# Kernel optimization log

Hardware: AMD Instinct MI355X
Metric: run time of the kernel (lower is better)

The kernel has to match this reference:

```python
import jax, jax.numpy as jnp
import numpy as np

H = 16          # num heads
D = 128         # head dim
WIN = 128       # local sliding window
EPS = 1e-6
ROPE_BASE = 500000.0


def rmsnorm(x, w, eps=EPS):
    var = jnp.mean(x * x, axis=-1, keepdims=True)
    return x * jax.lax.rsqrt(var + eps) * w


def rope(x, positions):
    # x: [T, H, D], neox-style rotate-halves
    half = D // 2
    inv_freq = 1.0 / (ROPE_BASE ** (jnp.arange(half, dtype=jnp.float32) / half * 2.0 / 2.0 * 2.0))
    inv_freq = 1.0 / (ROPE_BASE ** (jnp.arange(0, D, 2, dtype=jnp.float32) / D))
    ang = positions.astype(jnp.float32)[:, None] * inv_freq[None, :]      # [T, D/2]
    cos, sin = jnp.cos(ang)[:, None, :], jnp.sin(ang)[:, None, :]         # [T, 1, D/2]
    x1, x2 = x[..., :half], x[..., half:]
    return jnp.concatenate([x1 * cos - x2 * sin, x2 * cos + x1 * sin], axis=-1)


def attend(q, k, v, mask, scale):
    # q,k,v: [T, H, D]; mask: [T, T] (True = attend)
    scores = jnp.einsum('thd,shd->hts', q, k) * scale
    scores = jnp.where(mask[None], scores, jnp.finfo(scores.dtype).min)
    p = jax.nn.softmax(scores, axis=-1)
    return jnp.einsum('hts,shd->thd', p, v)


def setup_inputs() -> dict:
    key = jax.random.key(0)
    ks = jax.random.split(key, 8)
    T, hid = 2048, 2048
    s = 0.02
    return {
        'hidden_states': jax.random.normal(ks[0], (T, hid), jnp.float32),
        'positions': jnp.arange(T, dtype=jnp.int32),
        'Wq': jax.random.normal(ks[1], (hid, H * D + H), jnp.float32) * s,
        'Wk': jax.random.normal(ks[2], (hid, H * D), jnp.float32) * s,
        'Wv': jax.random.normal(ks[3], (hid, H * D), jnp.float32) * s,
        'Wo': jax.random.normal(ks[4], (H * D, hid), jnp.float32) * s,
        'q_norm_w': jnp.ones((hid,), jnp.float32),
        'k_norm_w': jnp.ones((H * D,), jnp.float32),
    }


def reference(hidden_states, positions, Wq, Wk, Wv, Wo, q_norm_w, k_norm_w):
    T = hidden_states.shape[0]
    scale = D ** -0.5
    qg = hidden_states @ Wq                             # [T, H*D + H]
    q, gate = qg[:, :H * D], qg[:, H * D:]              # [T, H*D], [T, H]
    k = hidden_states @ Wk
    v = hidden_states @ Wv
    q = rmsnorm(q, q_norm_w)
    k = rmsnorm(k, k_norm_w)
    q = rope(q.reshape(T, H, D), positions)
    k = rope(k.reshape(T, H, D), positions)
    v = v.reshape(T, H, D)
    # masks
    pi, pj = positions[:, None], positions[None, :]
    causal = pi >= pj
    local = causal & ((pi - pj) < WIN)
    global_out = attend(q, k, v, causal, scale)         # [T, H, D]
    local_out = attend(q, k, v, local, scale)           # [T, H, D]
    gate_hard = (jax.nn.sigmoid(gate) > 0.5).astype(hidden_states.dtype)[:, :, None]
    blended = global_out * gate_hard + local_out * (1.0 - gate_hard)
    return blended.reshape(T, H * D) @ Wo
```

## Files before the change

kernel.cpp:

```cpp
#include <hip/hip_runtime.h>

typedef _Float16 f16;
typedef __attribute__((ext_vector_type(8))) _Float16 half8;
typedef __attribute__((ext_vector_type(4))) _Float16 half4v;
typedef __attribute__((ext_vector_type(4))) float floatx4;

#define T_DIM 2048
#define HID   2048
#define NH    16
#define HD    128
#define QG_LD 2064
#define SM_SCALE 0.08838834764831845f
#define NEG_BIG  -1e30f

__device__ __forceinline__ void async16(const void* g, void* l) {
  __builtin_amdgcn_global_load_lds((const __attribute__((address_space(1))) void*)g,
                                   (__attribute__((address_space(3))) void*)l, 16, 0, 0);
}

__global__ __launch_bounds__(256) void transpose_all(const float* __restrict__ Wq,
                                                     const float* __restrict__ Wk,
                                                     const float* __restrict__ Wv,
                                                     f16* __restrict__ WqT, f16* __restrict__ WkT,
                                                     f16* __restrict__ WvT) {
  __shared__ float tile[32][33];
  const int z = blockIdx.z;
  const float* src = (z == 0) ? Wq : ((z == 1) ? Wk : Wv);
  const int ld = (z == 0) ? QG_LD : 2048;
  f16* dst = (z == 0) ? WqT : ((z == 1) ? WkT : WvT);
  const int bx = blockIdx.x * 32, by = blockIdx.y * 32;
  const int tx = threadIdx.x, ty = threadIdx.y;
#pragma unroll
  for (int i = 0; i < 4; ++i)
    tile[ty + 8 * i][tx] = src[(size_t)(by + ty + 8 * i) * ld + bx + tx];
  __syncthreads();
#pragma unroll
  for (int i = 0; i < 4; ++i)
    dst[(size_t)(bx + ty + 8 * i) * HID + by + tx] = (f16)tile[tx][ty + 8 * i];
}

__global__ __launch_bounds__(256) void transpose_w(const float* __restrict__ src, int src_ld,
                                                   f16* __restrict__ dst) {
  __shared__ float tile[32][33];
  const int bx = blockIdx.x * 32, by = blockIdx.y * 32;
  const int tx = threadIdx.x, ty = threadIdx.y;
#pragma unroll
  for (int i = 0; i < 4; ++i)
    tile[ty + 8 * i][tx] = src[(size_t)(by + ty + 8 * i) * src_ld + bx + tx];
  __syncthreads();
#pragma unroll
  for (int i = 0; i < 4; ++i)
    dst[(size_t)(bx + ty + 8 * i) * HID + by + tx] = (f16)tile[tx][ty + 8 * i];
}

__global__ __launch_bounds__(256) void transpose_h(const f16* __restrict__ src, f16* __restrict__ dst) {
  __shared__ f16 tile[32][33];
  const int bx = blockIdx.x * 32, by = blockIdx.y * 32;
  const int tx = threadIdx.x, ty = threadIdx.y;
#pragma unroll
  for (int i = 0; i < 4; ++i)
    tile[ty + 8 * i][tx] = src[(size_t)(by + ty + 8 * i) * T_DIM + bx + tx];
  __syncthreads();
#pragma unroll
  for (int i = 0; i < 4; ++i)
    dst[(size_t)(bx + ty + 8 * i) * T_DIM + by + tx] = tile[tx][ty + 8 * i];
}

__global__ __launch_bounds__(256) void convert_f32_f16(const float* __restrict__ src, f16* __restrict__ dst) {
  const int i = (blockIdx.x * 256 + threadIdx.x) * 4;
  const float4 v = *(const float4*)(src + i);
  half4v o;
  o.x = (f16)v.x; o.y = (f16)v.y; o.z = (f16)v.z; o.w = (f16)v.w;
  *(half4v*)(dst + i) = o;
}

__global__ __launch_bounds__(256) void gate_kernel(const float* __restrict__ hidden,
                                                   const float* __restrict__ Wq,
                                                   float* __restrict__ gate) {
  __shared__ double red[256][16];
  const int t = blockIdx.x, tid = threadIdx.x;
  double sums[16];
#pragma unroll
  for (int h2 = 0; h2 < 16; ++h2) sums[h2] = 0.0;
  const float* hrow = hidden + (size_t)t * HID;
  for (int k = tid; k < HID; k += 256) {
    const double hv = (double)hrow[k];
    const float* wr = Wq + (size_t)k * QG_LD + 2048;
#pragma unroll
    for (int h2 = 0; h2 < 16; ++h2) sums[h2] += hv * (double)wr[h2];
  }
#pragma unroll
  for (int h2 = 0; h2 < 16; ++h2) red[tid][h2] = sums[h2];
  __syncthreads();
  for (int st = 128; st > 0; st >>= 1) {
    if (tid < st) {
#pragma unroll
      for (int h2 = 0; h2 < 16; ++h2) red[tid][h2] += red[tid + st][h2];
    }
    __syncthreads();
  }
  if (tid < 16) gate[(size_t)t * 16 + tid] = (red[0][tid] > 0.0) ? 1.f : 0.f;
}

__global__ __launch_bounds__(256) void norm_rope2(const f16* __restrict__ qsrc, const f16* __restrict__ ksrc,
                                                  const float* __restrict__ qw, const float* __restrict__ kw,
                                                  const int* __restrict__ pos,
                                                  f16* __restrict__ qdst, f16* __restrict__ kdst) {
  __shared__ float row[2048];
  __shared__ float red[256];
  const int t = blockIdx.x & 2047, sel = blockIdx.x >> 11, tid = threadIdx.x;
  const f16* s = (sel ? ksrc : qsrc) + (size_t)t * HID;
  const float* w = sel ? kw : qw;
  f16* dst = sel ? kdst : qdst;
  float ss = 0.f;
#pragma unroll
  for (int e = 0; e < 8; ++e) {
    float v = (float)s[tid + 256 * e];
    row[tid + 256 * e] = v;
    ss += v * v;
  }
  red[tid] = ss;
  __syncthreads();
  for (int st = 128; st > 0; st >>= 1) {
    if (tid < st) red[tid] += red[tid + st];
    __syncthreads();
  }
  const float scl = rsqrtf(red[0] * (1.f / 2048.f) + 1e-6f);
  const float p = (float)pos[t];
#pragma unroll
  for (int e = 0; e < 8; ++e) {
    const int idx = tid + 256 * e;
    const int d = idx & 127;
    const int dh = d & 63;
    const int pidx = (d < 64) ? idx + 64 : idx - 64;
    const float xn = row[idx] * scl * w[idx];
    const float xp = row[pidx] * scl * w[pidx];
    const float inv = __expf(-(float)dh * 0.20503692772194388f);
    float cs, sn;
    sincosf(p * inv, &sn, &cs);
    const float o = (d < 64) ? (xn * cs - xp * sn) : (xn * cs + xp * sn);
    dst[(size_t)t * HID + idx] = (f16)o;
  }
}

__device__ __forceinline__ void gemm_issue(const f16* __restrict__ A, const f16* __restrict__ Bt,
                                           char* As, char* Bs, int m0, int n0, int k0,
                                           int wave, int srow, int scol) {
#pragma unroll
  for (int i = 0; i < 4; ++i) {
    async16(A + (size_t)(m0 + 32 * i + srow) * 2048 + k0 + scol, As + 4096 * i + 1024 * wave);
    async16(Bt + (size_t)(n0 + 32 * i + srow) * 2048 + k0 + scol, Bs + 4096 * i + 1024 * wave);
  }
}

__device__ __forceinline__ void gemm_core_db(const f16* __restrict__ A, const f16* __restrict__ Bt,
                                             f16* As, f16* Bs, floatx4 (&acc)[4][4],
                                             int kbase, int klen) {
  const int tid = threadIdx.x;
  const int lane = tid & 63, wave = tid >> 6;
  const int m0 = blockIdx.y * 128, n0 = blockIdx.x * 128;
  const int mo = (wave >> 1) * 64, no = (wave & 1) * 64;
  const int cn = lane & 15, q16 = lane >> 4;
  const int srow = 8 * wave + (lane >> 3);
  const int scol = (lane & 7) * 8;
  gemm_issue(A, Bt, (char*)As, (char*)Bs, m0, n0, kbase, wave, srow, scol);
  int cur = 0;
  for (int k0 = kbase; k0 < kbase + klen; k0 += 64) {
    __syncthreads();
    if (k0 + 64 < kbase + klen)
      gemm_issue(A, Bt, (char*)(As + (cur ^ 1) * 8192), (char*)(Bs + (cur ^ 1) * 8192),
                 m0, n0, k0 + 64, wave, srow, scol);
    const f16* as = As + cur * 8192;
    const f16* bs = Bs + cur * 8192;
#pragma unroll
    for (int kk = 0; kk < 64; kk += 32) {
      half8 av[4], bv[4];
#pragma unroll
      for (int i = 0; i < 4; ++i) av[i] = *(const half8*)&as[(mo + i * 16 + cn) * 64 + kk + q16 * 8];
#pragma unroll
      for (int i = 0; i < 4; ++i) bv[i] = *(const half8*)&bs[(no + i * 16 + cn) * 64 + kk + q16 * 8];
#pragma unroll
      for (int i = 0; i < 4; ++i)
#pragma unroll
        for (int j = 0; j < 4; ++j)
          acc[i][j] = __builtin_amdgcn_mfma_f32_16x16x32_f16(av[i], bv[j], acc[i][j], 0, 0, 0);
    }
    cur ^= 1;
  }
}

#define NKT 32

__device__ __forceinline__ void stage_half(const f16* __restrict__ src, int row0, int kcol,
                                           char* dst, int wv, int lane) {
  const int rsw = lane >> 3;
  const int csw = ((lane & 7) ^ rsw) << 3;
#pragma unroll
  for (int L = 0; L < 2; ++L)
    async16(src + (size_t)(row0 + L * 64 + wv * 8 + rsw) * 2048 + kcol + csw,
            dst + (L * 64 + wv * 8) * 128);
}

template <int MQ>
__device__ __forceinline__ void ld_a4(half8 (&a)[4][2], const f16* As, int wm, int cn, int q16) {
#pragma unroll
  for (int rf = 0; rf < 4; ++rf)
#pragma unroll
    for (int kh = 0; kh < 2; ++kh) {
      const int R = wm * 128 + MQ * 64 + rf * 16 + cn;
      a[rf][kh] = *(const half8*)&As[R * 64 + (((kh * 4 + q16) ^ (cn & 7)) << 3)];
    }
}

template <int NQ>
__device__ __forceinline__ void ld_b2(half8 (&b)[2][2], const f16* Bs, int wn, int cn, int q16) {
#pragma unroll
  for (int cf = 0; cf < 2; ++cf)
#pragma unroll
    for (int kh = 0; kh < 2; ++kh) {
      const int S = wn * 64 + NQ * 32 + cf * 16 + cn;
      b[cf][kh] = *(const half8*)&Bs[S * 64 + (((kh * 4 + q16) ^ (cn & 7)) << 3)];
    }
}

template <int MQ, int NQ>
__device__ __forceinline__ void mma16(floatx4 (&acc)[8][4], const half8 (&a)[4][2], const half8 (&b)[2][2]) {
#pragma unroll
  for (int kh = 0; kh < 2; ++kh)
#pragma unroll
    for (int rf = 0; rf < 4; ++rf)
#pragma unroll
      for (int cf = 0; cf < 2; ++cf)
        acc[MQ * 4 + rf][NQ * 2 + cf] = __builtin_amdgcn_mfma_f32_16x16x32_f16(
            a[rf][kh], b[cf][kh], acc[MQ * 4 + rf][NQ * 2 + cf], 0, 0, 0);
}

#define LGKM0() asm volatile("s_waitcnt lgkmcnt(0)" ::: "memory")
#define BAR()   __builtin_amdgcn_s_barrier()
#define PRIO(x) __builtin_amdgcn_s_setprio(x)
#define HBASE(p, isB, h) ((char*)lds + (p) * 65536 + (isB) * 32768 + (h) * 16384)

__global__ __launch_bounds__(512, 2) void gemm_qkv8(const f16* __restrict__ A,
                                                    const f16* __restrict__ B0_, const f16* __restrict__ B1_,
                                                    const f16* __restrict__ B2_,
                                                    f16* __restrict__ C0, f16* __restrict__ C1,
                                                    f16* __restrict__ C2) {
  __shared__ __align__(16) f16 lds[65536];
  const int tid = threadIdx.x;
  const int lane = tid & 63, wv = tid >> 6;
  const int wm = wv >> 2, wn = wv & 3;
  const int q16 = lane >> 4, cn = lane & 15;
  const int z = blockIdx.z;
  const f16* Bt = (z == 0) ? B0_ : ((z == 1) ? B1_ : B2_);
  f16* C = (z == 0) ? C0 : ((z == 1) ? C1 : C2);
  const int m0 = blockIdx.y * 256, n0 = blockIdx.x * 256;

  floatx4 acc[8][4] = {};
  half8 a[4][2], b0[2][2], b1[2][2];

  stage_half(A,  m0,       0,  HBASE(0, 0, 0), wv, lane);
  stage_half(Bt, n0,       0,  HBASE(0, 1, 0), wv, lane);
  stage_half(Bt, n0 + 128, 0,  HBASE(0, 1, 1), wv, lane);
  stage_half(A,  m0 + 128, 0,  HBASE(0, 0, 1), wv, lane);
  stage_half(Bt, n0,       64, HBASE(1, 1, 0), wv, lane);
  stage_half(A,  m0,       64, HBASE(1, 0, 0), wv, lane);
  asm volatile("s_waitcnt vmcnt(4)" ::: "memory");
  BAR();

  for (int t = 0; t < NKT; ++t) {
    const int pb = t & 1;
    const f16* As = lds + pb * 32768;
    const f16* Bs = As + 16384;
    ld_a4<0>(a, As, wm, cn, q16);
    ld_b2<0>(b0, Bs, wn, cn, q16);
    if (t + 1 < NKT) stage_half(Bt, n0 + 128, (t + 1) * 64, HBASE(pb ^ 1, 1, 1), wv, lane);
    LGKM0(); BAR();
    PRIO(1); mma16<0, 0>(acc, a, b0); PRIO(0);
    BAR();
    ld_b2<1>(b1, Bs, wn, cn, q16);
    if (t + 1 < NKT) stage_half(A, m0 + 128, (t + 1) * 64, HBASE(pb ^ 1, 0, 1), wv, lane);
    LGKM0(); BAR();
    PRIO(1); mma16<0, 1>(acc, a, b1); PRIO(0);
    BAR();
    ld_a4<1>(a, As, wm, cn, q16);
    if (t + 2 < NKT) stage_half(Bt, n0, (t + 2) * 64, HBASE(pb, 1, 0), wv, lane);
    LGKM0(); BAR();
    PRIO(1); mma16<1, 0>(acc, a, b0); PRIO(0);
    BAR();
    if (t + 2 < NKT) {
      stage_half(A, m0, (t + 2) * 64, HBASE(pb, 0, 0), wv, lane);
      asm volatile("s_waitcnt vmcnt(4)" ::: "memory");
    } else if (t == NKT - 2) {
      asm volatile("s_waitcnt vmcnt(0)" ::: "memory");
    }
    BAR();
    PRIO(1); mma16<1, 1>(acc, a, b1); PRIO(0);
    BAR();
  }

  const int r0 = q16 * 4;
#pragma unroll
  for (int i = 0; i < 8; ++i)
#pragma unroll
    for (int j = 0; j < 4; ++j)
#pragma unroll
      for (int r = 0; r < 4; ++r)
        C[(size_t)(m0 + wm * 128 + i * 16 + r0 + r) * 2048 + n0 + wn * 64 + j * 16 + cn] =
            (f16)acc[i][j][r];
}

__global__ __launch_bounds__(256, 2) void gemm_out_sk(const f16* __restrict__ A, const f16* __restrict__ Bt,
                                                      float* __restrict__ P0, float* __restrict__ P1) {
  __shared__ __align__(16) f16 As[2 * 128 * 64];
  __shared__ __align__(16) f16 Bs[2 * 128 * 64];
  const int z = blockIdx.z;
  floatx4 acc[4][4] = {};
  gemm_core_db(A, Bt, As, Bs, acc, z * 1024, 1024);
  float* C = z ? P1 : P0;
  const int lane = threadIdx.x & 63, wave = threadIdx.x >> 6;
  const int mb = blockIdx.y * 128 + (wave >> 1) * 64;
  const int nb = blockIdx.x * 128 + (wave & 1) * 64;
  const int r0 = (lane >> 4) * 4, cn = lane & 15;
#pragma unroll
  for (int i = 0; i < 4; ++i)
#pragma unroll
    for (int j = 0; j < 4; ++j)
#pragma unroll
      for (int r = 0; r < 4; ++r)
        C[(size_t)(mb + i * 16 + r0 + r) * 2048 + nb + j * 16 + cn] = acc[i][j][r];
}

__global__ __launch_bounds__(256) void add_out(const float* __restrict__ P0, const float* __restrict__ P1,
                                               float* __restrict__ out) {
  const int i = (blockIdx.x * 256 + threadIdx.x) * 4;
  const float4 a = *(const float4*)(P0 + i);
  const float4 b = *(const float4*)(P1 + i);
  float4 o;
  o.x = a.x + b.x; o.y = a.y + b.y; o.z = a.z + b.z; o.w = a.w + b.w;
  *(float4*)(out + i) = o;
}

__global__ __launch_bounds__(256, 2) void flash_kernel(const f16* __restrict__ Qg, const f16* __restrict__ Kg,
                                                       const f16* __restrict__ VTg, const float* __restrict__ gate,
                                                       f16* __restrict__ Oa) {
  __shared__ __align__(16) f16 Ks[2][64 * 128];
  __shared__ __align__(16) f16 VTs[2][128 * 64];
  __shared__ __align__(16) f16 Ps[4][16][72];

  const int tid = threadIdx.x;
  const int lane = tid & 63, wv = tid >> 6;
  const int q16 = lane >> 4, cn = lane & 15;
  const int r0 = q16 * 4;

  const int p = blockIdx.x;
  const int xcd = p & 7;
  const int idx = p >> 3;
  const int h = (xcd << 1) | (idx & 1);
  const int rest = idx >> 1;
  const int qt = (rest < 16) ? rest : 47 - rest;
  const int t0 = qt * 64;

  bool gbit[4];
#pragma unroll
  for (int r = 0; r < 4; ++r)
    gbit[r] = gate[(size_t)(t0 + wv * 16 + r0 + r) * NH + h] > 0.5f;

  half8 qa[4];
#pragma unroll
  for (int i = 0; i < 4; ++i)
    qa[i] = *(const half8*)(Qg + (size_t)(t0 + 16 * wv + cn) * HID + h * HD + 32 * i + q16 * 8);

#pragma unroll
  for (int i = 0; i < 4; ++i) {
    const int rk = 16 * i + 4 * wv + q16;
    async16(Kg + (size_t)rk * HID + h * HD + ((cn ^ (rk & 7)) << 3), (char*)Ks[0] + 4096 * i + 1024 * wv);
    const int rv = 32 * i + 8 * wv + (lane >> 3);
    async16(VTg + (size_t)(h * HD + rv) * T_DIM + (((lane & 7) ^ (lane >> 3)) << 3),
            (char*)VTs[0] + 4096 * i + 1024 * wv);
  }

  floatx4 og[8] = {};
  floatx4 lacc = {0.f, 0.f, 0.f, 0.f};
  float mg[4];
#pragma unroll
  for (int r = 0; r < 4; ++r) mg[r] = NEG_BIG;

  const half8 ones = {(f16)1, (f16)1, (f16)1, (f16)1, (f16)1, (f16)1, (f16)1, (f16)1};

  int cur = 0;
  for (int kt = 0; kt <= qt; ++kt) {
    const int s0 = kt * 64;
    __syncthreads();
    if (kt < qt) {
      const int sn = s0 + 64;
#pragma unroll
      for (int i = 0; i < 4; ++i) {
        const int rk = 16 * i + 4 * wv + q16;
        async16(Kg + (size_t)(sn + rk) * HID + h * HD + ((cn ^ (rk & 7)) << 3),
                (char*)Ks[cur ^ 1] + 4096 * i + 1024 * wv);
        const int rv = 32 * i + 8 * wv + (lane >> 3);
        async16(VTg + (size_t)(h * HD + rv) * T_DIM + sn + (((lane & 7) ^ (lane >> 3)) << 3),
                (char*)VTs[cur ^ 1] + 4096 * i + 1024 * wv);
      }
    }

    floatx4 sacc[4] = {};
    PRIO(1);
#pragma unroll
    for (int i = 0; i < 4; ++i)
#pragma unroll
      for (int nt = 0; nt < 4; ++nt) {
        half8 b = *(const half8*)&Ks[cur][(nt * 16 + cn) * 128 + (((4 * i + q16) ^ (cn & 7)) << 3)];
        sacc[nt] = __builtin_amdgcn_mfma_f32_16x16x32_f16(qa[i], b, sacc[nt], 0, 0, 0);
      }
    PRIO(0);

    const bool diag = (kt == qt);

    float pe[4][4];
#pragma unroll
    for (int nt = 0; nt < 4; ++nt)
#pragma unroll
      for (int r = 0; r < 4; ++r) {
        float x = sacc[nt][r] * SM_SCALE;
        if (diag && (s0 + nt * 16 + cn > t0 + wv * 16 + r0 + r)) x = NEG_BIG;
        pe[nt][r] = x;
      }

    float rmax[4];
#pragma unroll
    for (int r = 0; r < 4; ++r)
      rmax[r] = fmaxf(fmaxf(pe[0][r], pe[1][r]), fmaxf(pe[2][r], pe[3][r]));
#pragma unroll
    for (int off = 1; off < 16; off <<= 1)
#pragma unroll
      for (int r = 0; r < 4; ++r) rmax[r] = fmaxf(rmax[r], __shfl_xor(rmax[r], off, 64));

    float alpha[4];
#pragma unroll
    for (int r = 0; r < 4; ++r) {
      const float mn = fmaxf(mg[r], rmax[r]);
      alpha[r] = __expf(mg[r] - mn);
      mg[r] = mn;
    }
#pragma unroll
    for (int dt = 0; dt < 8; ++dt)
#pragma unroll
      for (int r = 0; r < 4; ++r) og[dt][r] *= alpha[r];
#pragma unroll
    for (int r = 0; r < 4; ++r) lacc[r] *= alpha[r];

#pragma unroll
    for (int nt = 0; nt < 4; ++nt)
#pragma unroll
      for (int r = 0; r < 4; ++r) {
        const float e = __expf(pe[nt][r] - mg[r]);
        const int tt = t0 + wv * 16 + r0 + r;
        const int s = s0 + nt * 16 + cn;
        const bool keep = gbit[r] || (tt - s < 128);
        Ps[wv][r0 + r][nt * 16 + cn] = keep ? (f16)e : (f16)0.f;
      }

    PRIO(1);
#pragma unroll
    for (int kk = 0; kk < 64; kk += 32) {
      half8 a = *(const half8*)&Ps[wv][cn][kk + q16 * 8];
#pragma unroll
      for (int dt = 0; dt < 8; ++dt) {
        half8 b = *(const half8*)&VTs[cur][(dt * 16 + cn) * 64 + ((((kk >> 3) + q16) ^ (cn & 7)) << 3)];
        og[dt] = __builtin_amdgcn_mfma_f32_16x16x32_f16(a, b, og[dt], 0, 0, 0);
      }
      lacc = __builtin_amdgcn_mfma_f32_16x16x32_f16(a, ones, lacc, 0, 0, 0);
    }
    PRIO(0);
    cur ^= 1;
  }

#pragma unroll
  for (int dt = 0; dt < 8; ++dt)
#pragma unroll
    for (int r = 0; r < 4; ++r) {
      const float v = og[dt][r] / lacc[r];
      Oa[(size_t)(t0 + wv * 16 + r0 + r) * HID + h * HD + dt * 16 + cn] = (f16)v;
    }
}

extern "C" void kernel_launch(void* const* d_in, const int* in_sizes, int n_in,
                              void* d_out, int out_size, void* d_ws, size_t ws_size,
                              hipStream_t stream) {
  const float* hidden = (const float*)d_in[0];
  const int* pos = (const int*)d_in[1];
  const float* Wq = (const float*)d_in[2];
  const float* Wk = (const float*)d_in[3];
  const float* Wv = (const float*)d_in[4];
  const float* Wo = (const float*)d_in[5];
  const float* qw = (const float*)d_in[6];
  const float* kw = (const float*)d_in[7];

  char* ws = (char*)d_ws;
  const size_t MB = 1ull << 20;
  f16* WqT = (f16*)(ws + 0 * MB);
  f16* WkT = (f16*)(ws + 8 * MB);
  f16* WvT = (f16*)(ws + 16 * MB);
  f16* hidh = (f16*)(ws + 24 * MB);
  f16* q_raw = (f16*)(ws + 32 * MB);
  f16* k_raw = (f16*)(ws + 48 * MB);
  f16* v_h = (f16*)(ws + 64 * MB);
  f16* q_h = (f16*)(ws + 72 * MB);
  f16* k_h = (f16*)(ws + 80 * MB);
  float* gate = (float*)(ws + 88 * MB);
  f16* WoT = WqT;
  f16* attn = q_raw;
  f16* vT = k_raw;
  float* P0 = (float*)(ws + 8 * MB);
  float* P1 = (float*)(ws + 72 * MB);

  dim3 tb(32, 8);
  transpose_all<<<dim3(64, 64, 3), tb, 0, stream>>>(Wq, Wk, Wv, WqT, WkT, WvT);
  convert_f32_f16<<<4096, 256, 0, stream>>>(hidden, hidh);
  gate_kernel<<<2048, 256, 0, stream>>>(hidden, Wq, gate);
  gemm_qkv8<<<dim3(8, 8, 3), 512, 0, stream>>>(hidh, WqT, WkT, WvT, q_raw, k_raw, v_h);
  transpose_w<<<dim3(64, 64), tb, 0, stream>>>(Wo, 2048, WoT);
  norm_rope2<<<4096, 256, 0, stream>>>(q_raw, k_raw, qw, kw, pos, q_h, k_h);
  transpose_h<<<dim3(64, 64), tb, 0, stream>>>(v_h, vT);
  flash_kernel<<<512, 256, 0, stream>>>(q_h, k_h, vT, gate, attn);
  gemm_out_sk<<<dim3(16, 16, 2), 256, 0, stream>>>(attn, WoT, P0, P1);
  add_out<<<4096, 256, 0, stream>>>(P0, P1, (float*)d_out);
}
```

Measured before the change: 346.7 us.

## Split long causal query tiles across blocks and merge partial softmax results

Result: no change. 348.7 us (+0.6%).

```diff
diff --git a/kernel.cpp b/kernel.cpp
--- a/kernel.cpp
+++ b/kernel.cpp
@@ -342,7 +342,8 @@
 
 __global__ __launch_bounds__(256, 2) void flash_kernel(const f16* __restrict__ Qg, const f16* __restrict__ Kg,
                                                        const f16* __restrict__ VTg, const float* __restrict__ gate,
-                                                       f16* __restrict__ Oa) {
+                                                       f16* __restrict__ Oa, float* __restrict__ Opart,
+                                                       float2* __restrict__ ml) {
   __shared__ __align__(16) f16 Ks[2][64 * 128];
   __shared__ __align__(16) f16 VTs[2][128 * 64];
   __shared__ __align__(16) f16 Ps[4][16][72];
@@ -353,11 +354,18 @@
   const int r0 = q16 * 4;
 
   const int p = blockIdx.x;
-  const int xcd = p & 7;
-  const int idx = p >> 3;
-  const int h = (xcd << 1) | (idx & 1);
-  const int rest = idx >> 1;
-  const int qt = (rest < 16) ? rest : 47 - rest;
+  const int o = p >> 4;
+  const int h = p & 15;
+  int qt, nsp, piece, slot_o;
+  if (o < 24)      { qt = 31 - o / 3;        nsp = 3; piece = o % 3;        slot_o = o; }
+  else if (o < 36) { qt = 35 - o;            nsp = 1; piece = 0;            slot_o = 0; }
+  else             { int u = o - 36; qt = 23 - (u >> 1); nsp = 2; piece = u & 1; slot_o = 24 + u; }
+  const int L = qt + 1;
+  const int base = L / nsp, rem = L % nsp;
+  const int kb = piece * base + (piece < rem ? piece : rem);
+  const int ke = kb + base + (piece < rem ? 1 : 0) - 1;
+  const bool split = (nsp > 1);
+  const int slot = h * 48 + slot_o;
   const int t0 = qt * 64;
 
   bool gbit[4];
@@ -370,13 +378,17 @@
   for (int i = 0; i < 4; ++i)
     qa[i] = *(const half8*)(Qg + (size_t)(t0 + 16 * wv + cn) * HID + h * HD + 32 * i + q16 * 8);
 
-#pragma unroll
-  for (int i = 0; i < 4; ++i) {
-    const int rk = 16 * i + 4 * wv + q16;
-    async16(Kg + (size_t)rk * HID + h * HD + ((cn ^ (rk & 7)) << 3), (char*)Ks[0] + 4096 * i + 1024 * wv);
-    const int rv = 32 * i + 8 * wv + (lane >> 3);
-    async16(VTg + (size_t)(h * HD + rv) * T_DIM + (((lane & 7) ^ (lane >> 3)) << 3),
-            (char*)VTs[0] + 4096 * i + 1024 * wv);
+  {
+    const int sb = kb * 64;
+#pragma unroll
+    for (int i = 0; i < 4; ++i) {
+      const int rk = 16 * i + 4 * wv + q16;
+      async16(Kg + (size_t)(sb + rk) * HID + h * HD + ((cn ^ (rk & 7)) << 3),
+              (char*)Ks[0] + 4096 * i + 1024 * wv);
+      const int rv = 32 * i + 8 * wv + (lane >> 3);
+      async16(VTg + (size_t)(h * HD + rv) * T_DIM + sb + (((lane & 7) ^ (lane >> 3)) << 3),
+              (char*)VTs[0] + 4096 * i + 1024 * wv);
+    }
   }
 
   floatx4 og[8] = {};
@@ -388,10 +400,10 @@
   const half8 ones = {(f16)1, (f16)1, (f16)1, (f16)1, (f16)1, (f16)1, (f16)1, (f16)1};
 
   int cur = 0;
-  for (int kt = 0; kt <= qt; ++kt) {
+  for (int kt = kb; kt <= ke; ++kt) {
     const int s0 = kt * 64;
     __syncthreads();
-    if (kt < qt) {
+    if (kt < ke) {
       const int sn = s0 + 64;
 #pragma unroll
       for (int i = 0; i < 4; ++i) {
@@ -436,19 +448,22 @@
 #pragma unroll
       for (int r = 0; r < 4; ++r) rmax[r] = fmaxf(rmax[r], __shfl_xor(rmax[r], off, 64));
 
-    float alpha[4];
-#pragma unroll
-    for (int r = 0; r < 4; ++r) {
-      const float mn = fmaxf(mg[r], rmax[r]);
-      alpha[r] = __expf(mg[r] - mn);
-      mg[r] = mn;
-    }
-#pragma unroll
-    for (int dt = 0; dt < 8; ++dt)
-#pragma unroll
-      for (int r = 0; r < 4; ++r) og[dt][r] *= alpha[r];
-#pragma unroll
-    for (int r = 0; r < 4; ++r) lacc[r] *= alpha[r];
+    const bool grow = (rmax[0] > mg[0]) | (rmax[1] > mg[1]) | (rmax[2] > mg[2]) | (rmax[3] > mg[3]);
+    if (__any(grow)) {
+      float alpha[4];
+#pragma unroll
+      for (int r = 0; r < 4; ++r) {
+        const float mn = fmaxf(mg[r], rmax[r]);
+        alpha[r] = __expf(mg[r] - mn);
+        mg[r] = mn;
+      }
+#pragma unroll
+      for (int dt = 0; dt < 8; ++dt)
+#pragma unroll
+        for (int r = 0; r < 4; ++r) og[dt][r] *= alpha[r];
+#pragma unroll
+      for (int r = 0; r < 4; ++r) lacc[r] *= alpha[r];
+    }
 
 #pragma unroll
     for (int nt = 0; nt < 4; ++nt)
@@ -476,13 +491,75 @@
     cur ^= 1;
   }
 
-#pragma unroll
-  for (int dt = 0; dt < 8; ++dt)
-#pragma unroll
-    for (int r = 0; r < 4; ++r) {
-      const float v = og[dt][r] / lacc[r];
-      Oa[(size_t)(t0 + wv * 16 + r0 + r) * HID + h * HD + dt * 16 + cn] = (f16)v;
-    }
+  if (!split) {
+#pragma unroll
+    for (int dt = 0; dt < 8; ++dt)
+#pragma unroll
+      for (int r = 0; r < 4; ++r) {
+        const float v = og[dt][r] / lacc[r];
+        Oa[(size_t)(t0 + wv * 16 + r0 + r) * HID + h * HD + dt * 16 + cn] = (f16)v;
+      }
+  } else {
+    float* ob = Opart + ((size_t)slot * 64 + wv * 16) * 128;
+#pragma unroll
+    for (int dt = 0; dt < 8; ++dt)
+#pragma unroll
+      for (int r = 0; r < 4; ++r)
+        ob[(r0 + r) * 128 + dt * 16 + cn] = og[dt][r];
+    if (cn == 0) {
+      float2* mlp = ml + slot * 64 + wv * 16;
+#pragma unroll
+      for (int r = 0; r < 4; ++r) mlp[r0 + r] = float2{mg[r], lacc[r]};
+    }
+  }
+}
+
+__global__ __launch_bounds__(256) void merge_chunks(const float* __restrict__ Opart,
+                                                    const float2* __restrict__ ml,
+                                                    f16* __restrict__ attn) {
+  const int b = blockIdx.x;
+  const int h = b & 15, v = b >> 4;
+  const int qt = 12 + v;
+  const int n = (qt >= 24) ? 3 : 2;
+  const int s0 = (qt >= 24) ? (h * 48 + 3 * (31 - qt)) : (h * 48 + 24 + 2 * (23 - qt));
+  const int tid = threadIdx.x;
+  const int row = tid >> 2;
+  const int cq = (tid & 3) * 32;
+
+  float m = NEG_BIG, mv[3], lv[3];
+#pragma unroll
+  for (int c = 0; c < 3; ++c) {
+    if (c < n) {
+      const float2 x = ml[(s0 + c) * 64 + row];
+      mv[c] = x.x; lv[c] = x.y;
+      m = fmaxf(m, x.x);
+    }
+  }
+  float e[3], denom = 0.f;
+#pragma unroll
+  for (int c = 0; c < 3; ++c) {
+    if (c < n) {
+      e[c] = __expf(mv[c] - m);
+      denom += e[c] * lv[c];
+    }
+  }
+  const float inv = 1.f / denom;
+  f16* out = attn + (size_t)(qt * 64 + row) * 2048 + h * 128 + cq;
+#pragma unroll
+  for (int i = 0; i < 32; i += 4) {
+    float4 acc = {0.f, 0.f, 0.f, 0.f};
+#pragma unroll
+    for (int c = 0; c < 3; ++c) {
+      if (c < n) {
+        const float4 a = *(const float4*)(Opart + ((size_t)(s0 + c) * 64 + row) * 128 + cq + i);
+        acc.x += e[c] * a.x; acc.y += e[c] * a.y; acc.z += e[c] * a.z; acc.w += e[c] * a.w;
+      }
+    }
+    out[i + 0] = (f16)(acc.x * inv);
+    out[i + 1] = (f16)(acc.y * inv);
+    out[i + 2] = (f16)(acc.z * inv);
+    out[i + 3] = (f16)(acc.w * inv);
+  }
 }
 
 extern "C" void kernel_launch(void* const* d_in, const int* in_sizes, int n_in,
@@ -514,6 +591,8 @@
   f16* vT = k_raw;
   float* P0 = (float*)(ws + 8 * MB);
   float* P1 = (float*)(ws + 72 * MB);
+  float* Opart = (float*)(ws + 8 * MB);
+  float2* mlbuf = (float2*)(ws + 40 * MB);
 
   dim3 tb(32, 8);
   transpose_all<<<dim3(64, 64, 3), tb, 0, stream>>>(Wq, Wk, Wv, WqT, WkT, WvT);
@@ -523,7 +602,8 @@
   transpose_w<<<dim3(64, 64), tb, 0, stream>>>(Wo, 2048, WoT);
   norm_rope2<<<4096, 256, 0, stream>>>(q_raw, k_raw, qw, kw, pos, q_h, k_h);
   transpose_h<<<dim3(64, 64), tb, 0, stream>>>(v_h, vT);
-  flash_kernel<<<512, 256, 0, stream>>>(q_h, k_h, vT, gate, attn);
+  flash_kernel<<<960, 256, 0, stream>>>(q_h, k_h, vT, gate, attn, Opart, mlbuf);
+  merge_chunks<<<320, 256, 0, stream>>>(Opart, mlbuf, attn);
   gemm_out_sk<<<dim3(16, 16, 2), 256, 0, stream>>>(attn, WoT, P0, P1);
   add_out<<<4096, 256, 0, stream>>>(P0, P1, (float*)d_out);
 }
```
